# Performance work log

Measured on AMD Instinct MI355X. Metric: run time of the kernel, lower is better.

## Reference

```python
import jax, jax.numpy as jnp
import numpy as np

EPS = 1e-5


def setup_inputs() -> dict:
    key = jax.random.key(0)
    k1, k2, k3, k4 = jax.random.split(key, 4)
    B, C_in, C_out, N_in = 4, 128, 256, 40962
    N_out = (N_in + 6) // 4  # 10242
    x = jax.random.normal(k1, (B, C_in, N_in), dtype=jnp.float32)
    neigh_orders = jax.random.randint(k2, (N_out * 7,), 0, N_in, dtype=jnp.int64)
    W = jax.random.normal(k3, (C_out, C_in), dtype=jnp.float32) * 0.05
    b = jax.random.normal(k4, (C_out,), dtype=jnp.float32) * 0.05
    gamma = jnp.ones((C_out,), dtype=jnp.float32)
    beta = jnp.zeros((C_out,), dtype=jnp.float32)
    return {"x": x, "neigh_orders": neigh_orders, "W": W, "b": b,
            "gamma": gamma, "beta": beta}


def reference(x, neigh_orders, W, b, gamma, beta):
    B, C, N_in = x.shape
    N_out = (N_in + 6) // 4
    idx = neigh_orders[: N_out * 7]
    # irregular gather: (B, C, N_out*7) -> (B, C, N_out, 7), mean over the 7 neighbors
    g = x[:, :, idx].reshape(B, C, N_out, 7).mean(axis=3)  # (B, C, N_out)
    # 1x1 conv == channel GEMM
    y = jnp.einsum('oc,bcn->bon', W, g) + b[None, :, None]  # (B, C_out, N_out)
    # BatchNorm1d with batch statistics (track_running_stats=False), biased var
    mean = y.mean(axis=(0, 2))
    var = y.var(axis=(0, 2))
    y = (y - mean[None, :, None]) * jax.lax.rsqrt(var[None, :, None] + EPS)
    return gamma[None, :, None] * y + beta[None, :, None]
```

## Files before the change

kernel.cpp:

```cpp
#include <hip/hip_runtime.h>
#include <hip/hip_bf16.h>

#define B_ 4
#define C_IN 128
#define C_OUT 256
#define N_IN 40962
#define N_OUT 10242
#define EPS_ 1e-5f

typedef __attribute__((ext_vector_type(8))) short bf16x8;
typedef __attribute__((ext_vector_type(4))) float f32x4;

__device__ __forceinline__ float bf2f(unsigned short u) {
    union { unsigned int i; float f; } c;
    c.i = ((unsigned int)u) << 16;
    return c.f;
}
__device__ __forceinline__ unsigned short f2bf(float f) {
    union { float f; unsigned int i; } c;
    c.f = f;
    unsigned int r = c.i + 0x7FFFu + ((c.i >> 16) & 1u);
    return (unsigned short)(r >> 16);
}

#define IBLK 64
#define NB_I ((N_IN + IBLK - 1) / IBLK)
#define WCONV_BLKS ((C_OUT * C_IN) / 256)

__global__ __launch_bounds__(256) void k_transpose(const float* __restrict__ x,
                                                   unsigned short* __restrict__ xT,
                                                   const float* __restrict__ W,
                                                   unsigned short* __restrict__ Wb) {
    if (blockIdx.x >= B_ * NB_I) {
        int i = (blockIdx.x - B_ * NB_I) * 256 + threadIdx.x;
        Wb[i] = f2bf(W[i]);
        return;
    }
    __shared__ float tile[IBLK][C_IN + 1];
    int b  = blockIdx.x / NB_I;
    int ib = blockIdx.x % NB_I;
    int i0 = ib * IBLK;
    int t = threadIdx.x;
    int lane = t & 63;
    int q = t >> 6;

    const float* xb = x + (size_t)b * C_IN * N_IN;
    int i = i0 + lane;
    if (i < N_IN) {
#pragma unroll
        for (int p = 0; p < 32; p++) {
            int k = p * 4 + q;
            tile[lane][k] = xb[(size_t)k * N_IN + i];
        }
    }
    __syncthreads();

    unsigned short* xTb = xT + (size_t)b * N_IN * C_IN;
#pragma unroll
    for (int p = 0; p < 16; p++) {
        int il = p * 4 + q;
        int gi = i0 + il;
        if (gi < N_IN) {
            int k2 = lane * 2;
            float a = tile[il][k2];
            float c = tile[il][k2 + 1];
            unsigned int pk = (unsigned int)f2bf(a) | ((unsigned int)f2bf(c) << 16);
            *reinterpret_cast<unsigned int*>(xTb + (size_t)gi * C_IN + k2) = pk;
        }
    }
}

#define GNB 16
#define NB_G ((N_OUT + GNB - 1) / GNB)

__global__ __launch_bounds__(256) void k_gather(const unsigned short* __restrict__ xT,
                                                const int* __restrict__ idx,
                                                unsigned short* __restrict__ g) {
    int b  = blockIdx.x / NB_G;
    int nb = blockIdx.x % NB_G;
    int t = threadIdx.x;
    int n = nb * GNB + (t >> 4);
    int c = t & 15;
    if (n >= N_OUT) return;

    const unsigned short* xTb = xT + (size_t)b * N_IN * C_IN;
    const int* ip = idx + 7 * n;
    float s[8];
#pragma unroll
    for (int e = 0; e < 8; e++) s[e] = 0.f;
#pragma unroll
    for (int j = 0; j < 7; j++) {
        int id = ip[j];
        bf16x8 v = *reinterpret_cast<const bf16x8*>(xTb + (size_t)id * C_IN + c * 8);
#pragma unroll
        for (int e = 0; e < 8; e++) s[e] += bf2f((unsigned short)v[e]);
    }
    const float inv7 = 1.0f / 7.0f;
    bf16x8 r;
#pragma unroll
    for (int e = 0; e < 8; e++) r[e] = (short)f2bf(s[e] * inv7);
    *reinterpret_cast<bf16x8*>(g + ((size_t)b * N_OUT + n) * C_IN + c * 8) = r;
}

#define NT2 64
#define NB_N2 ((N_OUT + NT2 - 1) / NT2)
#define NBLK_GS (B_ * NB_N2)

__global__ __launch_bounds__(256, 2) void k_stats_gemm(const unsigned short* __restrict__ g,
                                                       const unsigned short* __restrict__ Wb,
                                                       const float* __restrict__ bias,
                                                       float* __restrict__ psum) {
    int bid = blockIdx.x;
    int b  = bid / NB_N2;
    int nb = bid % NB_N2;
    int n0 = nb * NT2;
    int t = threadIdx.x;
    int w = t >> 6, l = t & 63, lr = l & 15, lg = l >> 4;
    int wbase = w * 64;

    bf16x8 afrag[4][4];
#pragma unroll
    for (int mt = 0; mt < 4; mt++)
#pragma unroll
        for (int ks = 0; ks < 4; ks++)
            afrag[mt][ks] = *reinterpret_cast<const bf16x8*>(
                Wb + (size_t)(wbase + mt * 16 + lr) * C_IN + ks * 32 + lg * 8);

    f32x4 acc[4][4];
#pragma unroll
    for (int mt = 0; mt < 4; mt++)
#pragma unroll
        for (int nt = 0; nt < 4; nt++) acc[mt][nt] = (f32x4)(0.0f);

    const unsigned short* gb = g + (size_t)b * N_OUT * C_IN;
#pragma unroll
    for (int nt = 0; nt < 4; nt++) {
        int n = n0 + nt * 16 + lr;
        const unsigned short* gr = gb + (size_t)((n < N_OUT) ? n : 0) * C_IN;
#pragma unroll
        for (int ks = 0; ks < 4; ks++) {
            bf16x8 bfr = *reinterpret_cast<const bf16x8*>(gr + ks * 32 + lg * 8);
#pragma unroll
            for (int mt = 0; mt < 4; mt++)
                acc[mt][nt] = __builtin_amdgcn_mfma_f32_16x16x32_bf16(afrag[mt][ks], bfr,
                                                                     acc[mt][nt], 0, 0, 0);
        }
    }

    float ps1[16], ps2[16];
#pragma unroll
    for (int m = 0; m < 16; m++) { ps1[m] = 0.f; ps2[m] = 0.f; }
#pragma unroll
    for (int mt = 0; mt < 4; mt++) {
#pragma unroll
        for (int j = 0; j < 4; j++) {
            int o = wbase + mt * 16 + lg * 4 + j;
            float bv = bias[o];
#pragma unroll
            for (int nt = 0; nt < 4; nt++) {
                int n = n0 + nt * 16 + lr;
                if (n < N_OUT) {
                    float v = acc[mt][nt][j] + bv;
                    ps1[mt * 4 + j] += v;
                    ps2[mt * 4 + j] += v * v;
                }
            }
        }
    }

    __shared__ float red[2][C_OUT];
#pragma unroll
    for (int m = 0; m < 16; m++) {
        float a = ps1[m], cc = ps2[m];
#pragma unroll
        for (int d = 1; d < 16; d <<= 1) {
            a  += __shfl_xor(a, d, 64);
            cc += __shfl_xor(cc, d, 64);
        }
        if (lr == 0) {
            int mt = m >> 2, j = m & 3;
            int o = wbase + mt * 16 + lg * 4 + j;
            red[0][o] = a;
            red[1][o] = cc;
        }
    }
    __syncthreads();
    float* pb = psum + (size_t)bid * 2 * C_OUT;
    pb[t] = red[0][t];
    pb[C_OUT + t] = red[1][t];
}

#define RED_BLKS 32
__global__ __launch_bounds__(256) void k_reduce(const float* __restrict__ psum,
                                                float* __restrict__ psum2) {
    int r = blockIdx.x;
    int t = threadIdx.x;
    float a = 0.f, c = 0.f;
    for (int i = r; i < NBLK_GS; i += RED_BLKS) {
        const float* pb = psum + (size_t)i * 2 * C_OUT;
        a += pb[t];
        c += pb[C_OUT + t];
    }
    float* qb = psum2 + (size_t)r * 2 * C_OUT;
    qb[t] = a;
    qb[C_OUT + t] = c;
}

__global__ void k_finalize(const float* __restrict__ psum2, const float* __restrict__ bias,
                           const float* __restrict__ gamma, const float* __restrict__ beta,
                           float* __restrict__ ss) {
    int o = threadIdx.x;
    float s1 = 0.f, s2 = 0.f;
#pragma unroll 4
    for (int r = 0; r < RED_BLKS; r++) {
        s1 += psum2[(size_t)r * 2 * C_OUT + o];
        s2 += psum2[(size_t)r * 2 * C_OUT + C_OUT + o];
    }
    const float cnt = (float)(B_ * N_OUT);
    float mean = s1 / cnt;
    float var = s2 / cnt - mean * mean;
    float a = gamma[o] * rsqrtf(var + EPS_);
    ss[o] = a;
    ss[C_OUT + o] = a * bias[o] + beta[o] - a * mean;
}

__global__ __launch_bounds__(256, 2) void k_final_gemm(const unsigned short* __restrict__ g,
                                                       const unsigned short* __restrict__ Wb,
                                                       const float* __restrict__ ss,
                                                       float* __restrict__ out) {
    int b  = blockIdx.x / NB_N2;
    int nb = blockIdx.x % NB_N2;
    int n0 = nb * NT2;
    int t = threadIdx.x;
    int w = t >> 6, l = t & 63, lr = l & 15, lg = l >> 4;
    int wbase = w * 64;

    bf16x8 afrag[4][4];
#pragma unroll
    for (int mt = 0; mt < 4; mt++)
#pragma unroll
        for (int ks = 0; ks < 4; ks++)
            afrag[mt][ks] = *reinterpret_cast<const bf16x8*>(
                Wb + (size_t)(wbase + mt * 16 + lr) * C_IN + ks * 32 + lg * 8);

    f32x4 acc[4][4];
#pragma unroll
    for (int mt = 0; mt < 4; mt++)
#pragma unroll
        for (int nt = 0; nt < 4; nt++) acc[mt][nt] = (f32x4)(0.0f);

    const unsigned short* gb = g + (size_t)b * N_OUT * C_IN;
#pragma unroll
    for (int nt = 0; nt < 4; nt++) {
        int n = n0 + nt * 16 + lr;
        const unsigned short* gr = gb + (size_t)((n < N_OUT) ? n : 0) * C_IN;
#pragma unroll
        for (int ks = 0; ks < 4; ks++) {
            bf16x8 bfr = *reinterpret_cast<const bf16x8*>(gr + ks * 32 + lg * 8);
#pragma unroll
            for (int mt = 0; mt < 4; mt++)
                acc[mt][nt] = __builtin_amdgcn_mfma_f32_16x16x32_bf16(afrag[mt][ks], bfr,
                                                                     acc[mt][nt], 0, 0, 0);
        }
    }

    float* ob = out + (size_t)b * C_OUT * N_OUT;
#pragma unroll
    for (int mt = 0; mt < 4; mt++) {
#pragma unroll
        for (int j = 0; j < 4; j++) {
            int o = wbase + mt * 16 + lg * 4 + j;
            float a = ss[o];
            float sh = ss[C_OUT + o];
#pragma unroll
            for (int nt = 0; nt < 4; nt++) {
                int n = n0 + nt * 16 + lr;
                if (n < N_OUT) ob[(size_t)o * N_OUT + n] = a * acc[mt][nt][j] + sh;
            }
        }
    }
}

extern "C" void kernel_launch(void* const* d_in, const int* in_sizes, int n_in,
                              void* d_out, int out_size, void* d_ws, size_t ws_size,
                              hipStream_t stream) {
    const float* x     = (const float*)d_in[0];
    const int*   idx   = (const int*)d_in[1];
    const float* W     = (const float*)d_in[2];
    const float* bias  = (const float*)d_in[3];
    const float* gamma = (const float*)d_in[4];
    const float* beta  = (const float*)d_in[5];
    float* out = (float*)d_out;

    const size_t xt_bytes = (size_t)B_ * N_IN * C_IN * sizeof(unsigned short);
    const size_t g_bytes  = (size_t)B_ * N_OUT * C_IN * sizeof(unsigned short);
    const size_t wb_bytes = (size_t)C_OUT * C_IN * sizeof(unsigned short);
    unsigned short* xT = (unsigned short*)d_ws;
    unsigned short* gg = (unsigned short*)((char*)d_ws + xt_bytes);
    unsigned short* Wb = (unsigned short*)((char*)d_ws + xt_bytes + g_bytes);
    float* psum  = (float*)((char*)d_ws + xt_bytes + g_bytes + wb_bytes);
    float* psum2 = psum + (size_t)NBLK_GS * 2 * C_OUT;
    float* ss    = psum2 + (size_t)RED_BLKS * 2 * C_OUT;

    k_transpose<<<B_ * NB_I + WCONV_BLKS, 256, 0, stream>>>(x, xT, W, Wb);
    k_gather<<<B_ * NB_G, 256, 0, stream>>>(xT, idx, gg);
    k_stats_gemm<<<NBLK_GS, 256, 0, stream>>>(gg, Wb, bias, psum);
    k_reduce<<<RED_BLKS, 256, 0, stream>>>(psum, psum2);
    k_finalize<<<1, C_OUT, 0, stream>>>(psum2, bias, gamma, beta, ss);
    k_final_gemm<<<B_ * NB_N2, 256, 0, stream>>>(gg, Wb, ss, out);
}
```

Measured before the change: 93.50 us.

## Fuse neighbor gather with batch-stats GEMM into one kernel

Merges the gather kernel and the statistics GEMM kernel. Each block gathers 16 output vertices into shared memory, writes them to global for the final GEMM, and immediately runs the MFMA stats pass on the LDS tile. This avoids a kernel launch and a second global read of the gathered tensor. In exchange, the W fragments are re-read from global/L2 by four times as many blocks, and the partial-sum buffer and the later reduction grow by the same factor.

```diff
diff --git a/kernel.cpp b/kernel.cpp
--- a/kernel.cpp
+++ b/kernel.cpp
@@ -72,103 +72,89 @@
 
 #define GNB 16
 #define NB_G ((N_OUT + GNB - 1) / GNB)
-
-__global__ __launch_bounds__(256) void k_gather(const unsigned short* __restrict__ xT,
+#define NBLK_GS (B_ * NB_G)
+#define LROW (C_IN + 8)
+
+__global__ __launch_bounds__(256) void k_gstats(const unsigned short* __restrict__ xT,
                                                 const int* __restrict__ idx,
-                                                unsigned short* __restrict__ g) {
-    int b  = blockIdx.x / NB_G;
-    int nb = blockIdx.x % NB_G;
-    int t = threadIdx.x;
-    int n = nb * GNB + (t >> 4);
-    int c = t & 15;
-    if (n >= N_OUT) return;
+                                                const unsigned short* __restrict__ Wb,
+                                                const float* __restrict__ bias,
+                                                unsigned short* __restrict__ g,
+                                                float* __restrict__ psum) {
+    __shared__ unsigned short gl[GNB][LROW];
+    __shared__ float red[2][C_OUT];
+    int bid = blockIdx.x;
+    int b  = bid / NB_G;
+    int nb = bid % NB_G;
+    int n0 = nb * GNB;
+    int t = threadIdx.x;
+    int grp = t >> 4, c = t & 15;
 
     const unsigned short* xTb = xT + (size_t)b * N_IN * C_IN;
-    const int* ip = idx + 7 * n;
-    float s[8];
-#pragma unroll
-    for (int e = 0; e < 8; e++) s[e] = 0.f;
-#pragma unroll
-    for (int j = 0; j < 7; j++) {
-        int id = ip[j];
-        bf16x8 v = *reinterpret_cast<const bf16x8*>(xTb + (size_t)id * C_IN + c * 8);
-#pragma unroll
-        for (int e = 0; e < 8; e++) s[e] += bf2f((unsigned short)v[e]);
-    }
-    const float inv7 = 1.0f / 7.0f;
-    bf16x8 r;
-#pragma unroll
-    for (int e = 0; e < 8; e++) r[e] = (short)f2bf(s[e] * inv7);
-    *reinterpret_cast<bf16x8*>(g + ((size_t)b * N_OUT + n) * C_IN + c * 8) = r;
-}
-
-#define NT2 64
-#define NB_N2 ((N_OUT + NT2 - 1) / NT2)
-#define NBLK_GS (B_ * NB_N2)
-
-__global__ __launch_bounds__(256, 2) void k_stats_gemm(const unsigned short* __restrict__ g,
-                                                       const unsigned short* __restrict__ Wb,
-                                                       const float* __restrict__ bias,
-                                                       float* __restrict__ psum) {
-    int bid = blockIdx.x;
-    int b  = bid / NB_N2;
-    int nb = bid % NB_N2;
-    int n0 = nb * NT2;
-    int t = threadIdx.x;
+
+    {
+        int n = n0 + grp;
+        int nc = (n < N_OUT) ? n : (N_OUT - 1);
+        const int* ip = idx + 7 * nc;
+        float s[8];
+#pragma unroll
+        for (int e = 0; e < 8; e++) s[e] = 0.f;
+#pragma unroll
+        for (int j = 0; j < 7; j++) {
+            int id = ip[j];
+            bf16x8 v = *reinterpret_cast<const bf16x8*>(xTb + (size_t)id * C_IN + c * 8);
+#pragma unroll
+            for (int e = 0; e < 8; e++) s[e] += bf2f((unsigned short)v[e]);
+        }
+        const float inv7 = 1.0f / 7.0f;
+        bf16x8 r;
+#pragma unroll
+        for (int e = 0; e < 8; e++) r[e] = (short)f2bf(s[e] * inv7);
+        *reinterpret_cast<bf16x8*>(&gl[grp][c * 8]) = r;
+        if (n < N_OUT)
+            *reinterpret_cast<bf16x8*>(g + ((size_t)b * N_OUT + n) * C_IN + c * 8) = r;
+    }
+    __syncthreads();
+
     int w = t >> 6, l = t & 63, lr = l & 15, lg = l >> 4;
     int wbase = w * 64;
 
-    bf16x8 afrag[4][4];
-#pragma unroll
-    for (int mt = 0; mt < 4; mt++)
-#pragma unroll
-        for (int ks = 0; ks < 4; ks++)
-            afrag[mt][ks] = *reinterpret_cast<const bf16x8*>(
-                Wb + (size_t)(wbase + mt * 16 + lr) * C_IN + ks * 32 + lg * 8);
-
-    f32x4 acc[4][4];
-#pragma unroll
-    for (int mt = 0; mt < 4; mt++)
-#pragma unroll
-        for (int nt = 0; nt < 4; nt++) acc[mt][nt] = (f32x4)(0.0f);
-
-    const unsigned short* gb = g + (size_t)b * N_OUT * C_IN;
-#pragma unroll
-    for (int nt = 0; nt < 4; nt++) {
-        int n = n0 + nt * 16 + lr;
-        const unsigned short* gr = gb + (size_t)((n < N_OUT) ? n : 0) * C_IN;
+    bf16x8 bfr[4];
+#pragma unroll
+    for (int ks = 0; ks < 4; ks++)
+        bfr[ks] = *reinterpret_cast<const bf16x8*>(&gl[lr][ks * 32 + lg * 8]);
+
+    f32x4 acc[4];
+#pragma unroll
+    for (int mt = 0; mt < 4; mt++) acc[mt] = (f32x4)(0.0f);
+
+#pragma unroll
+    for (int mt = 0; mt < 4; mt++) {
+        const unsigned short* wr = Wb + (size_t)(wbase + mt * 16 + lr) * C_IN;
 #pragma unroll
         for (int ks = 0; ks < 4; ks++) {
-            bf16x8 bfr = *reinterpret_cast<const bf16x8*>(gr + ks * 32 + lg * 8);
-#pragma unroll
-            for (int mt = 0; mt < 4; mt++)
-                acc[mt][nt] = __builtin_amdgcn_mfma_f32_16x16x32_bf16(afrag[mt][ks], bfr,
-                                                                     acc[mt][nt], 0, 0, 0);
+            bf16x8 af = *reinterpret_cast<const bf16x8*>(wr + ks * 32 + lg * 8);
+            acc[mt] = __builtin_amdgcn_mfma_f32_16x16x32_bf16(af, bfr[ks], acc[mt], 0, 0, 0);
         }
     }
 
     float ps1[16], ps2[16];
 #pragma unroll
     for (int m = 0; m < 16; m++) { ps1[m] = 0.f; ps2[m] = 0.f; }
+    int n = n0 + lr;
+    bool nok = (n < N_OUT);
 #pragma unroll
     for (int mt = 0; mt < 4; mt++) {
 #pragma unroll
         for (int j = 0; j < 4; j++) {
             int o = wbase + mt * 16 + lg * 4 + j;
-            float bv = bias[o];
-#pragma unroll
-            for (int nt = 0; nt < 4; nt++) {
-                int n = n0 + nt * 16 + lr;
-                if (n < N_OUT) {
-                    float v = acc[mt][nt][j] + bv;
-                    ps1[mt * 4 + j] += v;
-                    ps2[mt * 4 + j] += v * v;
-                }
+            if (nok) {
+                float v = acc[mt][j] + bias[o];
+                ps1[mt * 4 + j] = v;
+                ps2[mt * 4 + j] = v * v;
             }
         }
     }
-
-    __shared__ float red[2][C_OUT];
 #pragma unroll
     for (int m = 0; m < 16; m++) {
         float a = ps1[m], cc = ps2[m];
@@ -223,6 +209,9 @@
     ss[o] = a;
     ss[C_OUT + o] = a * bias[o] + beta[o] - a * mean;
 }
+
+#define NT2 64
+#define NB_N2 ((N_OUT + NT2 - 1) / NT2)
 
 __global__ __launch_bounds__(256, 2) void k_final_gemm(const unsigned short* __restrict__ g,
                                                        const unsigned short* __restrict__ Wb,
@@ -303,8 +292,7 @@
     float* ss    = psum2 + (size_t)RED_BLKS * 2 * C_OUT;
 
     k_transpose<<<B_ * NB_I + WCONV_BLKS, 256, 0, stream>>>(x, xT, W, Wb);
-    k_gather<<<B_ * NB_G, 256, 0, stream>>>(xT, idx, gg);
-    k_stats_gemm<<<NBLK_GS, 256, 0, stream>>>(gg, Wb, bias, psum);
+    k_gstats<<<NBLK_GS, 256, 0, stream>>>(xT, idx, Wb, bias, gg, psum);
     k_reduce<<<RED_BLKS, 256, 0, stream>>>(psum, psum2);
     k_finalize<<<1, C_OUT, 0, stream>>>(psum2, bias, gamma, beta, ss);
     k_final_gemm<<<B_ * NB_N2, 256, 0, stream>>>(gg, Wb, ss, out);
```

Measured after the change: 120.9 us. 1.29x slower.
